# Kernel optimization log

Measured on AMD Instinct MI355X. Metric: run time of the kernel, lower is better.

Reference implementation:

```python
import jax, jax.numpy as jnp
import numpy as np
from jax import lax

EPS = 1e-3  # BatchNorm1d eps from norm_fn
SPARSE_SHAPE = (41, 200, 176)  # (z, y, x)
IN_CH = 4


def _conv3d(x, w, stride, pad):
    # x: [N,C,D,H,W], w: [O,I,kd,kh,kw]
    return lax.conv_general_dilated(x, w, window_strides=stride, padding=pad,
                                    dimension_numbers=('NCDHW', 'OIDHW', 'NCDHW'))


def _bn_relu(y, bn, mask):
    # eval-mode BatchNorm1d over active voxels == per-channel affine; inactive sites
    # must stay exactly 0 in a sparse tensor, hence the final mask multiply.
    g, b, m, v = bn[0], bn[1], bn[2], bn[3]
    scale = g * lax.rsqrt(v + EPS)
    shift = b - m * scale
    y = y * scale[None, :, None, None, None] + shift[None, :, None, None, None]
    return jax.nn.relu(y) * mask


def _subm(x, mask, w, bn):
    # SubMConv3d: conv evaluated only at existing active sites; active set unchanged.
    kd, kh, kw = w.shape[2:]
    pad = [(kd // 2, kd // 2), (kh // 2, kh // 2), (kw // 2, kw // 2)]
    return _bn_relu(_conv3d(x, w, (1, 1, 1), pad), bn, mask)


def _spconv(x, mask, w, bn, stride, pad):
    # SparseConv3d: output active set = sites with >=1 active input in receptive field.
    pads = [(p, p) for p in pad]
    y = _conv3d(x, w, stride, pads)
    k = tuple(w.shape[2:])
    new_mask = lax.reduce_window(mask, 0.0, lax.max, (1, 1) + k, (1, 1) + tuple(stride),
                                 [(0, 0), (0, 0)] + pads)
    new_mask = (new_mask > 0).astype(x.dtype)
    return _bn_relu(y, bn, new_mask), new_mask


def setup_inputs() -> dict:
    key = jax.random.key(0)
    ks = jax.random.split(key, 16)
    D, H, W = SPARSE_SHAPE
    mask = (jax.random.uniform(ks[0], (1, 1, D, H, W)) < 0.02).astype(jnp.float32)
    x = jax.random.normal(ks[1], (1, IN_CH, D, H, W), jnp.float32) * mask
    specs = [(16, IN_CH, (3, 3, 3)), (16, 16, (3, 3, 3)),
             (32, 16, (3, 3, 3)), (32, 32, (3, 3, 3)), (32, 32, (3, 3, 3)),
             (64, 32, (3, 3, 3)), (64, 64, (3, 3, 3)), (64, 64, (3, 3, 3)),
             (64, 64, (3, 3, 3)), (64, 64, (3, 3, 3)), (64, 64, (3, 3, 3)),
             (128, 64, (3, 1, 1))]
    inp = {'x': x, 'mask': mask}
    for i, (co, ci, k) in enumerate(specs):
        kk = jax.random.fold_in(ks[2], i)
        fan = ci * k[0] * k[1] * k[2]
        inp['w%d' % i] = jax.random.normal(kk, (co, ci) + k, jnp.float32) / np.sqrt(fan).astype(np.float32)
        inp['bn%d' % i] = jnp.stack([
            jax.random.uniform(jax.random.fold_in(kk, 1), (co,), minval=0.5, maxval=1.5),
            jax.random.normal(jax.random.fold_in(kk, 2), (co,)) * 0.1,
            jax.random.normal(jax.random.fold_in(kk, 3), (co,)) * 0.1,
            jax.random.uniform(jax.random.fold_in(kk, 4), (co,), minval=0.5, maxval=1.5)])
    return inp


def reference(x, mask, w0, bn0, w1, bn1, w2, bn2, w3, bn3, w4, bn4, w5, bn5,
              w6, bn6, w7, bn7, w8, bn8, w9, bn9, w10, bn10, w11, bn11):
    h = _subm(x, mask, w0, bn0)                       # conv_input (subm1)
    h = _subm(h, mask, w1, bn1)                       # conv1 -> x_conv1
    h, m2 = _spconv(h, mask, w2, bn2, (2, 2, 2), (1, 1, 1))  # conv2 down
    h = _subm(h, m2, w3, bn3)
    h = _subm(h, m2, w4, bn4)                         # x_conv2
    h, m3 = _spconv(h, m2, w5, bn5, (2, 2, 2), (1, 1, 1))    # conv3 down
    h = _subm(h, m3, w6, bn6)
    h = _subm(h, m3, w7, bn7)                         # x_conv3
    h, m4 = _spconv(h, m3, w8, bn8, (2, 2, 2), (0, 1, 1))    # conv4 down
    h = _subm(h, m4, w9, bn9)
    h = _subm(h, m4, w10, bn10)                       # x_conv4
    out, _ = _spconv(h, m4, w11, bn11, (2, 1, 1), (0, 0, 0)) # conv_out
    N, C, Dd, Hh, Ww = out.shape                      # [1,128,2,25,22]
    return out.reshape(N, C * Dd, Hh, Ww)             # spatial_features [1,256,25,22]
```

## Files before the change

kernel.cpp:

```cpp
#include <hip/hip_runtime.h>

#define BS 256

constexpr int D1=41, H1=200, W1=176; constexpr int N1v=D1*H1*W1;
constexpr int D2=21, H2=100, W2=88;  constexpr int N2v=D2*H2*W2;
constexpr int D3=11, H3=50,  W3=44;  constexpr int N3v=D3*H3*W3;
constexpr int D4=5,  H4=25,  W4=22;  constexpr int N4v=D4*H4*W4;
constexpr int DOo=2, HOo=25, WOo=22;
constexpr int ROWS1=40960;

typedef __attribute__((ext_vector_type(8))) short bf16x8;
typedef __attribute__((ext_vector_type(4))) float f32x4;

__device__ __forceinline__ float bflo(unsigned int u){ return __uint_as_float(u<<16); }
__device__ __forceinline__ float bfhi(unsigned int u){ return __uint_as_float(u & 0xffff0000u); }
__device__ __forceinline__ unsigned short f2bf(float f){
  unsigned int x = __float_as_uint(f);
  x += 0x7fffu + ((x>>16)&1u);
  return (unsigned short)(x>>16);
}
__device__ __forceinline__ void acc8(float& acc, uint4 p, const float* __restrict__ wk, int stride){
  acc = fmaf(bflo(p.x), wk[0*stride], acc);
  acc = fmaf(bfhi(p.x), wk[1*stride], acc);
  acc = fmaf(bflo(p.y), wk[2*stride], acc);
  acc = fmaf(bfhi(p.y), wk[3*stride], acc);
  acc = fmaf(bflo(p.z), wk[4*stride], acc);
  acc = fmaf(bfhi(p.z), wk[5*stride], acc);
  acc = fmaf(bflo(p.w), wk[6*stride], acc);
  acc = fmaf(bfhi(p.w), wk[7*stride], acc);
}

struct PrepArgs {
  const float* w[12]; const float* bn[12];
  void* dst[12]; float* bias[12];
  int O[12], I[12], K[12], mode[12];
  int off[13];
};

__global__ void prep_and_list_kernel(PrepArgs a, int prepB,
                                     const float* __restrict__ mask,
                                     const float* __restrict__ x,
                                     unsigned short* __restrict__ xcl,
                                     int* __restrict__ I1, int* __restrict__ list1,
                                     int* __restrict__ cnt, float* __restrict__ m2){
  if ((int)blockIdx.x < prepB){
    int t = blockIdx.x*BS + threadIdx.x;
    if (t >= a.off[12]) return;
    int li = 0;
    while (t >= a.off[li+1]) li++;
    int e = t - a.off[li];
    int O=a.O[li], I=a.I[li], K=a.K[li], mode=a.mode[li];
    const float* w = a.w[li]; const float* bn = a.bn[li];
    if (mode == 2){
      int p = e/(O*32); int rem = e - p*(O*32); int o = rem>>5; int kk = rem&31;
      int tap = 2*p + (kk>=16 ? 1 : 0); int ci = kk&15;
      float g=bn[o], b=bn[O+o], m=bn[2*O+o], v=bn[3*O+o];
      float sc = g*rsqrtf(v+1e-3f);
      float val = (tap < 27) ? w[(o*I+ci)*K + tap]*sc : 0.f;
      ((unsigned short*)a.dst[li])[e] = f2bf(val);
      if (p==0 && kk==0) a.bias[li][o] = b - m*sc;
    } else if (mode == 3){
      int ci = e % I; int tmp = e / I; int dx = tmp % 3; tmp /= 3; int o = tmp % O; int g9 = tmp / O;
      float g=bn[o], b=bn[O+o], m=bn[2*O+o], v=bn[3*O+o];
      float sc = g*rsqrtf(v+1e-3f);
      int tap = g9*3 + dx;
      ((unsigned short*)a.dst[li])[e] = f2bf(w[(o*I+ci)*27 + tap]*sc);
      if (g9==0 && dx==0 && ci==0) a.bias[li][o] = b - m*sc;
    } else {
      int k = e % K; int rest = e / K; int ci = rest % I; int o = rest / I;
      float g=bn[o], b=bn[O+o], m=bn[2*O+o], v=bn[3*O+o];
      float sc = g*rsqrtf(v+1e-3f);
      ((float*)a.dst[li])[(k*I+ci)*O + o] = w[(o*I+ci)*K + k]*sc;
      if (ci==0 && k==0) a.bias[li][o] = b - m*sc;
    }
    return;
  }
  constexpr int PER = 16;
  __shared__ int sc_[BS]; __shared__ int sbase;
  int b = blockIdx.x - prepB, t = threadIdx.x;
  int base_s = b*BS*PER;
  unsigned int bits = 0; int c = 0;
  #pragma unroll
  for (int i=0;i<PER;i++){
    int s = base_s + i*BS + t;
    bool act = false;
    if (s < N1v){
      act = mask[s] > 0.f;
      unsigned short h0 = f2bf(x[s]),       h1 = f2bf(x[N1v+s]);
      unsigned short h2 = f2bf(x[2*N1v+s]), h3 = f2bf(x[3*N1v+s]);
      uint2 pk; pk.x = ((unsigned)h1<<16)|h0; pk.y = ((unsigned)h3<<16)|h2;
      *(uint2*)(xcl + (size_t)s*4) = pk;
    }
    bits |= (act?1u:0u) << i; c += act;
  }
  sc_[t] = c;
  __syncthreads();
  for (int ofs=1; ofs<BS; ofs<<=1){
    int v = (t>=ofs) ? sc_[t-ofs] : 0;
    __syncthreads();
    sc_[t] += v;
    __syncthreads();
  }
  if (t == BS-1) sbase = atomicAdd(cnt, sc_[t]);
  __syncthreads();
  int pos = sbase + sc_[t] - c;
  #pragma unroll
  for (int i=0;i<PER;i++){
    if (bits & (1u<<i)){
      int s = base_s + i*BS + t;
      list1[pos] = s; I1[s] = pos+1; pos++;
      int zz = s/(H1*W1); int rem = s - zz*(H1*W1); int yy = rem/W1; int xx = rem - yy*W1;
      int az = zz+1, ay = yy+1, ax = xx+1;
      int zlo = (az-2) <= 0 ? 0 : (az-1)/2;  int zhi = min(D2-1, az/2);
      int ylo = (ay-2) <= 0 ? 0 : (ay-1)/2;  int yhi = min(H2-1, ay/2);
      int xlo = (ax-2) <= 0 ? 0 : (ax-1)/2;  int xhi = min(W2-1, ax/2);
      for (int zo=zlo; zo<=zhi; zo++)
        for (int yo=ylo; yo<=yhi; yo++)
          for (int xo=xlo; xo<=xhi; xo++)
            m2[(zo*H2+yo)*W2+xo] = 1.f;
    }
  }
}

template<int N,int HI,int WI,int DON,int HON,int WON,int PZ,int PY,int PX,bool SCAT>
__global__ void compact_mask_kernel(const float* __restrict__ mout,
                                    int* __restrict__ list, int* __restrict__ cnt1,
                                    float* __restrict__ mnext){
  __shared__ int sc[BS]; __shared__ int sbase;
  int b = blockIdx.x, t = threadIdx.x;
  int s = b*BS + t;
  bool act = (s < N) && (mout[s] > 0.f);
  int c = act ? 1 : 0;
  sc[t] = c;
  __syncthreads();
  for (int ofs=1; ofs<BS; ofs<<=1){
    int v = (t>=ofs) ? sc[t-ofs] : 0;
    __syncthreads();
    sc[t] += v;
    __syncthreads();
  }
  if (t == BS-1) sbase = atomicAdd(cnt1, sc[t]);
  __syncthreads();
  if (act){
    list[sbase + sc[t] - 1] = s;
    if (SCAT){
      int zz = s/(HI*WI); int rem = s - zz*(HI*WI); int yy = rem/WI; int xx = rem - yy*WI;
      int az = zz+PZ, ay = yy+PY, ax = xx+PX;
      int zlo = (az-2) <= 0 ? 0 : (az-1)/2;  int zhi = min(DON-1, az/2);
      int ylo = (ay-2) <= 0 ? 0 : (ay-1)/2;  int yhi = min(HON-1, ay/2);
      int xlo = (ax-2) <= 0 ? 0 : (ax-1)/2;  int xhi = min(WON-1, ax/2);
      for (int zo=zlo; zo<=zhi; zo++)
        for (int yo=ylo; yo<=yhi; yo++)
          for (int xo=xlo; xo<=xhi; xo++)
            mnext[(zo*HON+yo)*WON+xo] = 1.f;
    }
  }
}

__global__ void subm_l0_kernel(const unsigned short* __restrict__ xcl,
                               const int* __restrict__ list1, const int* __restrict__ cnt,
                               const float* __restrict__ wt, const float* __restrict__ bias,
                               unsigned short* __restrict__ fout){
  __shared__ float Wl[27*4*16];
  __shared__ float Bl[16];
  int t = threadIdx.x;
  for (int e=t; e<27*4*16; e+=BS) Wl[e] = wt[e];
  if (t < 16) Bl[t] = bias[t];
  __syncthreads();
  int row = blockIdx.x*BS + t;
  if (row >= cnt[0]) return;
  int s = list1[row];
  int z = s/(H1*W1); int r = s - z*(H1*W1); int y = r/W1; int xx = r - y*W1;
  float acc[16];
  #pragma unroll
  for (int o=0;o<16;o++) acc[o] = Bl[o];
  #pragma unroll
  for (int dz=-1; dz<=1; dz++){ int zz=z+dz; if ((unsigned)zz >= (unsigned)D1) continue;
    #pragma unroll
    for (int dy=-1; dy<=1; dy++){ int yy=y+dy; if ((unsigned)yy >= (unsigned)H1) continue;
      #pragma unroll
      for (int dx=-1; dx<=1; dx++){ int xc=xx+dx; if ((unsigned)xc >= (unsigned)W1) continue;
        int ns = (zz*H1+yy)*W1+xc;
        int k = ((dz+1)*3+(dy+1))*3+(dx+1);
        uint2 pk = *(const uint2*)(xcl + (size_t)ns*4);
        float x0 = bflo(pk.x), x1 = bfhi(pk.x), x2 = bflo(pk.y), x3 = bfhi(pk.y);
        const float* wk = Wl + k*64;
        #pragma unroll
        for (int o=0;o<16;o++)
          acc[o] = fmaf(x0, wk[o], fmaf(x1, wk[16+o], fmaf(x2, wk[32+o], fmaf(x3, wk[48+o], acc[o]))));
      }}}
  #pragma unroll
  for (int o=0;o<16;o++) fout[row*16+o] = f2bf(fmaxf(acc[o], 0.f));
}

template<int COUT,int HO,int WO,int PZ,int PY,int PX,int STR,bool DENSE_OUT>
__global__ __launch_bounds__(256)
void conv_mfma_l1_kernel(const unsigned short* __restrict__ fin,
                         const int* __restrict__ I1,
                         const int* __restrict__ list, const int* __restrict__ cnt, int cidx,
                         const unsigned short* __restrict__ wbt,
                         const float* __restrict__ bias,
                         unsigned short* __restrict__ outp){
  constexpr int BP = 40;
  constexpr int NT = COUT/16;
  __shared__ __align__(16) unsigned short B[14*COUT*BP];

  int nrows = cnt[cidx];
  int row0 = blockIdx.x*64;
  if (row0 >= nrows) return;

  int t = threadIdx.x;
  int lane = t & 63, wave = t >> 6;
  int m = lane & 15, quad = lane >> 4;

  constexpr int TOT = 14*COUT*32;
  for (int e = t*8; e < TOT; e += BS*8){
    int n = e >> 5, c = e & 31;
    *(uint4*)(&B[n*BP + c]) = *(const uint4*)(wbt + e);
  }

  int row = row0 + wave*16 + m;
  bool rv = row < nrows;
  int z=0, y=0, x=0;
  {
    int s = list[rv ? row : row0];
    z = s/(HO*WO); int rem = s - z*(HO*WO); y = rem/WO; x = rem - y*WO;
  }

  int rr[14];
  #pragma unroll
  for (int p=0;p<14;p++){
    int tap = 2*p + (quad>>1);
    rr[p] = 0;
    if (rv && tap < 27){
      int dz = tap/9, rem = tap - dz*9, dy = rem/3, dx = rem - dy*3;
      int zz = STR*z - PZ + dz, yy = STR*y - PY + dy, xx = STR*x - PX + dx;
      if ((unsigned)zz < (unsigned)D1 && (unsigned)yy < (unsigned)H1 && (unsigned)xx < (unsigned)W1)
        rr[p] = I1[(zz*H1+yy)*W1+xx];
    }
  }
  __syncthreads();

  f32x4 acc[NT];
  #pragma unroll
  for (int i=0;i<NT;i++) acc[i] = (f32x4){0.f,0.f,0.f,0.f};

  bf16x8 acur = (bf16x8){0,0,0,0,0,0,0,0};
  if (rr[0] > 0) acur = *(const bf16x8*)(fin + (size_t)(rr[0]-1)*16 + (quad&1)*8);
  #pragma unroll
  for (int p=0;p<14;p++){
    bf16x8 anext = (bf16x8){0,0,0,0,0,0,0,0};
    if (p < 13 && rr[p+1] > 0)
      anext = *(const bf16x8*)(fin + (size_t)(rr[p+1]-1)*16 + (quad&1)*8);
    #pragma unroll
    for (int nt=0; nt<NT; nt++){
      bf16x8 b = *(const bf16x8*)(&B[(p*COUT + nt*16 + m)*BP + quad*8]);
      acc[nt] = __builtin_amdgcn_mfma_f32_16x16x32_bf16(acur, b, acc[nt], 0, 0, 0);
    }
    acur = anext;
  }

  #pragma unroll
  for (int nt=0; nt<NT; nt++){
    int cout = nt*16 + m;
    float bv = bias[cout];
    #pragma unroll
    for (int rg=0; rg<4; rg++){
      int rw = row0 + wave*16 + quad*4 + rg;
      if (rw < nrows){
        float v = fmaxf(acc[nt][rg] + bv, 0.f);
        if (DENSE_OUT){
          int s = list[rw];
          outp[(size_t)s*COUT + cout] = f2bf(v);
        } else {
          outp[(size_t)rw*COUT + cout] = f2bf(v);
        }
      }
    }
  }
}

template<int CIN,int COUT,int DI,int HI,int WI,int HO,int WO,int PZ,int PY,int PX,int STR>
__global__ __launch_bounds__(256)
void conv_mfma2_kernel(const unsigned short* __restrict__ gin,
                       const int* __restrict__ list, const int* __restrict__ cnt, int cidx,
                       const unsigned short* __restrict__ wg,
                       const float* __restrict__ bias,
                       unsigned short* __restrict__ gout){
  constexpr int KW = 3*CIN;
  constexpr int BP = KW + 8;
  constexpr int NT = COUT/16;
  constexpr int KT = KW/32;
  constexpr int PREN = (COUT*KW + BS*8 - 1)/(BS*8);
  __shared__ __align__(16) unsigned short B[2][COUT*BP];

  int nrows = cnt[cidx];
  int row0 = blockIdx.x*64;
  if (row0 >= nrows) return;

  int t = threadIdx.x;
  int lane = t & 63, wave = t >> 6;
  int m = lane & 15, quad = lane >> 4;

  #pragma unroll
  for (int i=0;i<PREN;i++){
    int e = t*8 + i*BS*8;
    if (e < COUT*KW){
      int n = e / KW, c = e - n*KW;
      *(uint4*)(&B[0][n*BP + c]) = *(const uint4*)(wg + e);
    }
  }

  int row = row0 + wave*16 + m;
  bool rv = row < nrows;
  int z=0, y=0, x=0;
  {
    int s = list[rv ? row : row0];
    z = s/(HO*WO); int rem = s - z*(HO*WO); y = rem/WO; x = rem - y*WO;
  }

  auto loadA = [&](int g, bf16x8* av){
    int dz = g/3, dy = g - dz*3;
    int zz = STR*z - PZ + dz, yy = STR*y - PY + dy, xx0 = STR*x - PX;
    bool zyok = rv && (unsigned)zz < (unsigned)DI && (unsigned)yy < (unsigned)HI;
    int base = ((zz*HI + yy)*WI + xx0)*CIN;
    #pragma unroll
    for (int kt=0; kt<KT; kt++){
      int tapx = (kt*32)/CIN;
      av[kt] = (bf16x8){0,0,0,0,0,0,0,0};
      if (zyok && (unsigned)(xx0 + tapx) < (unsigned)WI)
        av[kt] = *(const bf16x8*)(gin + (size_t)(base + kt*32 + quad*8));
    }
  };

  f32x4 acc[NT];
  #pragma unroll
  for (int i=0;i<NT;i++) acc[i] = (f32x4){0.f,0.f,0.f,0.f};

  bf16x8 acur[KT], anext[KT];
  loadA(0, acur);
  __syncthreads();

  #pragma unroll
  for (int g=0; g<9; g++){
    uint4 pre[PREN];
    if (g < 8){
      const unsigned short* src = wg + (size_t)(g+1)*COUT*KW;
      #pragma unroll
      for (int i=0;i<PREN;i++){
        int e = t*8 + i*BS*8;
        pre[i] = (e < COUT*KW) ? *(const uint4*)(src + e) : (uint4){0,0,0,0};
      }
      loadA(g+1, anext);
    }
    #pragma unroll
    for (int kt=0; kt<KT; kt++){
      #pragma unroll
      for (int nt=0; nt<NT; nt++){
        bf16x8 b = *(const bf16x8*)(&B[g&1][(nt*16 + m)*BP + kt*32 + quad*8]);
        acc[nt] = __builtin_amdgcn_mfma_f32_16x16x32_bf16(acur[kt], b, acc[nt], 0, 0, 0);
      }
    }
    if (g < 8){
      #pragma unroll
      for (int i=0;i<PREN;i++){
        int e = t*8 + i*BS*8;
        if (e < COUT*KW){
          int n = e / KW, c = e - n*KW;
          *(uint4*)(&B[(g+1)&1][n*BP + c]) = pre[i];
        }
      }
      #pragma unroll
      for (int kt=0; kt<KT; kt++) acur[kt] = anext[kt];
    }
    __syncthreads();
  }

  #pragma unroll
  for (int nt=0; nt<NT; nt++){
    int cout = nt*16 + m;
    float bv = bias[cout];
    #pragma unroll
    for (int rg=0; rg<4; rg++){
      int rw = row0 + wave*16 + quad*4 + rg;
      if (rw < nrows){
        int s = list[rw];
        gout[(size_t)s*COUT + cout] = f2bf(fmaxf(acc[nt][rg] + bv, 0.f));
      }
    }
  }
}

template<int CIN,int COUT,int DI,int HI,int WI,int HO,int WO,int PZ,int PY,int PX,int STR>
__global__ __launch_bounds__(256)
void conv_tp_kernel(const unsigned short* __restrict__ gin,
                    const int* __restrict__ list, const int* __restrict__ cnt, int cidx,
                    const unsigned short* __restrict__ wg,
                    const float* __restrict__ bias,
                    unsigned short* __restrict__ gout){
  constexpr int KW = 3*CIN;
  constexpr int NT = COUT/16;
  constexpr int KT = KW/32;
  __shared__ float R[4][NT*256];

  int nrows = cnt[cidx];
  int row0 = blockIdx.x*16;
  if (row0 >= nrows) return;

  int t = threadIdx.x;
  int lane = t & 63, wave = t >> 6;
  int m = lane & 15, quad = lane >> 4;

  int row = row0 + m;
  bool rv = row < nrows;
  int z=0, y=0, x=0;
  {
    int s = list[rv ? row : row0];
    z = s/(HO*WO); int rem = s - z*(HO*WO); y = rem/WO; x = rem - y*WO;
  }

  bf16x8 av[3][KT];
  #pragma unroll
  for (int i=0;i<3;i++){
    int g = wave + i*4;
    #pragma unroll
    for (int kt=0; kt<KT; kt++) av[i][kt] = (bf16x8){0,0,0,0,0,0,0,0};
    if (g < 9){
      int dz = g/3, dy = g - dz*3;
      int zz = STR*z - PZ + dz, yy = STR*y - PY + dy, xx0 = STR*x - PX;
      bool zyok = rv && (unsigned)zz < (unsigned)DI && (unsigned)yy < (unsigned)HI;
      int base = ((zz*HI + yy)*WI + xx0)*CIN;
      #pragma unroll
      for (int kt=0; kt<KT; kt++){
        int tapx = (kt*32)/CIN;
        if (zyok && (unsigned)(xx0 + tapx) < (unsigned)WI)
          av[i][kt] = *(const bf16x8*)(gin + (size_t)(base + kt*32 + quad*8));
      }
    }
  }

  f32x4 acc[NT];
  #pragma unroll
  for (int i=0;i<NT;i++) acc[i] = (f32x4){0.f,0.f,0.f,0.f};

  #pragma unroll
  for (int i=0;i<3;i++){
    int g = wave + i*4;
    if (g < 9){
      const unsigned short* wsrc = wg + (size_t)g*COUT*KW;
      #pragma unroll
      for (int kt=0; kt<KT; kt++){
        #pragma unroll
        for (int nt=0; nt<NT; nt++){
          bf16x8 b = *(const bf16x8*)(wsrc + (size_t)(nt*16 + m)*KW + kt*32 + quad*8);
          acc[nt] = __builtin_amdgcn_mfma_f32_16x16x32_bf16(av[i][kt], b, acc[nt], 0, 0, 0);
        }
      }
    }
  }

  #pragma unroll
  for (int nt=0; nt<NT; nt++)
    #pragma unroll
    for (int rg=0; rg<4; rg++)
      R[wave][nt*256 + (quad*4+rg)*16 + m] = acc[nt][rg];
  __syncthreads();

  for (int e = t; e < 16*COUT; e += BS){
    int r = e / COUT, cout = e % COUT;
    int nt = cout >> 4, mm = cout & 15;
    int idx = nt*256 + r*16 + mm;
    float sum = R[0][idx] + R[1][idx] + R[2][idx] + R[3][idx];
    int rw = row0 + r;
    if (rw < nrows){
      int s = list[rw];
      gout[(size_t)s*COUT + cout] = f2bf(fmaxf(sum + bias[cout], 0.f));
    }
  }
}

__global__ void conv_out_kernel(const unsigned short* __restrict__ g4,
                                const float* __restrict__ m4,
                                const float* __restrict__ wt, const float* __restrict__ bias,
                                float* __restrict__ out){
  int t = blockIdx.x*BS + threadIdx.x;
  if (t >= 128*DOo*HOo*WOo) return;
  int cout = t & 127; int s = t >> 7;
  int d = s/(HOo*WOo); int r = s - d*(HOo*WOo); int h = r/WOo; int w = r - h*WOo;
  float res = 0.f;
  bool act = false;
  float acc = bias[cout];
  for (int dz=0; dz<3; dz++){
    int z4 = 2*d + dz;
    int site = (z4*H4 + h)*W4 + w;
    if (m4[site] == 0.f) continue;
    act = true;
    const uint4* fr = (const uint4*)(g4 + (size_t)site*64);
    const float* wk = wt + dz*64*128 + cout;
    #pragma unroll
    for (int q=0; q<8; q++) acc8(acc, fr[q], wk + q*8*128, 128);
  }
  if (act) res = fmaxf(acc, 0.f);
  out[((cout*DOo + d)*HOo + h)*WOo + w] = res;
}

extern "C" void kernel_launch(void* const* d_in, const int* in_sizes, int n_in,
                              void* d_out, int out_size, void* d_ws, size_t ws_size,
                              hipStream_t stream){
  const float* x    = (const float*)d_in[0];
  const float* mask = (const float*)d_in[1];
  const float* w[12]; const float* bnp[12];
  for (int i=0;i<12;i++){ w[i]=(const float*)d_in[2+2*i]; bnp[i]=(const float*)d_in[3+2*i]; }

  char* base = (char*)d_ws; size_t off = 0;
  auto alloc = [&](size_t b)->void*{ void* p = base + off; off = (off + b + 255) & ~(size_t)255; return p; };

  int* cnt   = (int*)alloc(16);
  int* I1    = (int*)alloc((size_t)N1v*4);
  unsigned short* g2a = (unsigned short*)alloc((size_t)N2v*32*2);
  unsigned short* g2b = (unsigned short*)alloc((size_t)N2v*32*2);
  unsigned short* g3a = (unsigned short*)alloc((size_t)N3v*64*2);
  unsigned short* g3b = (unsigned short*)alloc((size_t)N3v*64*2);
  unsigned short* g4a = (unsigned short*)alloc((size_t)N4v*64*2);
  unsigned short* g4b = (unsigned short*)alloc((size_t)N4v*64*2);
  float* m2 = (float*)alloc((size_t)N2v*4);
  float* m3 = (float*)alloc((size_t)N3v*4);
  float* m4 = (float*)alloc((size_t)N4v*4);
  size_t zero_bytes = off;
  unsigned short* xcl = (unsigned short*)alloc((size_t)N1v*4*2);
  int* list1 = (int*)alloc((size_t)ROWS1*4);
  unsigned short* f1a = (unsigned short*)alloc((size_t)ROWS1*16*2);
  unsigned short* f1b = (unsigned short*)alloc((size_t)ROWS1*16*2);
  int* list2 = (int*)alloc((size_t)N2v*4);
  int* list3 = (int*)alloc((size_t)N3v*4);
  int* list4 = (int*)alloc((size_t)N4v*4);

  static const int Oa[12]={16,16,32,32,32,64,64,64,64,64,64,128};
  static const int Ia[12]={ 4,16,16,32,32,32,64,64,64,64,64, 64};
  static const int Ka[12]={27,27,27,27,27,27,27,27,27,27,27,  3};
  static const int Ma[12]={ 0, 2, 2, 3, 3, 3, 3, 3, 3, 3, 3,  0};
  float* wt[12]; float* bs[12]; unsigned short* wbt[12];
  for (int i=0;i<12;i++){
    bs[i] = (float*)alloc((size_t)Oa[i]*4);
    wt[i]=nullptr; wbt[i]=nullptr;
    if (Ma[i]==0)      wt[i]  = (float*)alloc((size_t)Oa[i]*Ia[i]*Ka[i]*4);
    else if (Ma[i]==3) wbt[i] = (unsigned short*)alloc((size_t)Oa[i]*Ia[i]*27*2);
    else               wbt[i] = (unsigned short*)alloc((size_t)14*Oa[i]*32*2);
  }

  hipMemsetAsync(base, 0, zero_bytes, stream);

  PrepArgs pa;
  pa.off[0] = 0;
  for (int i=0;i<12;i++){
    pa.w[i]=w[i]; pa.bn[i]=bnp[i]; pa.bias[i]=bs[i];
    pa.O[i]=Oa[i]; pa.I[i]=Ia[i]; pa.K[i]=Ka[i]; pa.mode[i]=Ma[i];
    pa.dst[i] = (Ma[i]==0) ? (void*)wt[i] : (void*)wbt[i];
    int tot = (Ma[i]==2) ? 14*Oa[i]*32 : Oa[i]*Ia[i]*Ka[i];
    pa.off[i+1] = pa.off[i] + tot;
  }
  int prepB = (pa.off[12]+BS-1)/BS;
  int listB = (N1v + BS*16 - 1)/(BS*16);
  prep_and_list_kernel<<<prepB + listB, BS, 0, stream>>>(pa, prepB, mask, x, xcl, I1, list1, cnt, m2);

  subm_l0_kernel<<<(ROWS1+BS-1)/BS, BS, 0, stream>>>(xcl, list1, cnt, wt[0], bs[0], f1a);
  conv_mfma_l1_kernel<16,H1,W1,1,1,1,1,false><<<ROWS1/64, 256, 0, stream>>>
      (f1a, I1, list1, cnt, 0, wbt[1], bs[1], f1b);

  compact_mask_kernel<N2v,H2,W2,D3,H3,W3,1,1,1,true><<<(N2v+BS-1)/BS, BS, 0, stream>>>(m2, list2, cnt+1, m3);
  conv_mfma_l1_kernel<32,H2,W2,1,1,1,2,true><<<(N2v+63)/64, 256, 0, stream>>>
      (f1b, I1, list2, cnt, 1, wbt[2], bs[2], g2a);

  {
    int nb = (N2v + 63)/64;
    conv_mfma2_kernel<32,32,D2,H2,W2,H2,W2,1,1,1,1><<<nb, 256, 0, stream>>>(g2a, list2, cnt, 1, wbt[3], bs[3], g2b);
    conv_mfma2_kernel<32,32,D2,H2,W2,H2,W2,1,1,1,1><<<nb, 256, 0, stream>>>(g2b, list2, cnt, 1, wbt[4], bs[4], g2a);
  }

  compact_mask_kernel<N3v,H3,W3,D4,H4,W4,0,1,1,true><<<(N3v+BS-1)/BS, BS, 0, stream>>>(m3, list3, cnt+2, m4);
  {
    conv_tp_kernel<32,64,D2,H2,W2,H3,W3,1,1,1,2><<<(N3v+15)/16, 256, 0, stream>>>(g2a, list3, cnt, 2, wbt[5], bs[5], g3a);
    int nb = (N3v + 63)/64;
    conv_mfma2_kernel<64,64,D3,H3,W3,H3,W3,1,1,1,1><<<nb, 256, 0, stream>>>(g3a, list3, cnt, 2, wbt[6], bs[6], g3b);
    conv_mfma2_kernel<64,64,D3,H3,W3,H3,W3,1,1,1,1><<<nb, 256, 0, stream>>>(g3b, list3, cnt, 2, wbt[7], bs[7], g3a);
  }

  compact_mask_kernel<N4v,H4,W4,1,1,1,0,0,0,false><<<(N4v+BS-1)/BS, BS, 0, stream>>>(m4, list4, cnt+3, nullptr);
  {
    int nb = (N4v + 15)/16;
    conv_tp_kernel<64,64,D3,H3,W3,H4,W4,0,1,1,2><<<nb, 256, 0, stream>>>(g3a, list4, cnt, 3, wbt[8], bs[8], g4a);
    conv_tp_kernel<64,64,D4,H4,W4,H4,W4,1,1,1,1><<<nb, 256, 0, stream>>>(g4a, list4, cnt, 3, wbt[9], bs[9], g4b);
    conv_tp_kernel<64,64,D4,H4,W4,H4,W4,1,1,1,1><<<nb, 256, 0, stream>>>(g4b, list4, cnt, 3, wbt[10], bs[10], g4a);
  }

  conv_out_kernel<<<(128*DOo*HOo*WOo)/BS, BS, 0, stream>>>(g4a, m4, wt[11], bs[11], (float*)d_out);
}
```

Before: 360.5 us.

## Use single-wave blocks with register-streamed weights for early sparse convs

Replaces the 256-thread MFMA conv kernels for layers 1-4 with 64-thread single-wave kernels that each process 16 rows. Weight fragments come straight from global memory (through cache) into registers and are double-buffered, so the shared-memory weight staging and the __syncthreads are gone. The aim is to drop the per-block LDS fill cost and give finer-grained blocks for sparse, variable row counts. In exchange, every wave reloads the full weights from cache, many more blocks are launched, and register pressure rises from the double buffers.

```diff
diff --git a/kernel.cpp b/kernel.cpp
--- a/kernel.cpp
+++ b/kernel.cpp
@@ -194,32 +194,22 @@
 }
 
 template<int COUT,int HO,int WO,int PZ,int PY,int PX,int STR,bool DENSE_OUT>
-__global__ __launch_bounds__(256)
-void conv_mfma_l1_kernel(const unsigned short* __restrict__ fin,
-                         const int* __restrict__ I1,
-                         const int* __restrict__ list, const int* __restrict__ cnt, int cidx,
-                         const unsigned short* __restrict__ wbt,
-                         const float* __restrict__ bias,
-                         unsigned short* __restrict__ outp){
-  constexpr int BP = 40;
+__global__ __launch_bounds__(64)
+void conv_w1_kernel(const unsigned short* __restrict__ fin,
+                    const int* __restrict__ I1,
+                    const int* __restrict__ list, const int* __restrict__ cnt, int cidx,
+                    const unsigned short* __restrict__ wbt,
+                    const float* __restrict__ bias,
+                    unsigned short* __restrict__ outp){
   constexpr int NT = COUT/16;
-  __shared__ __align__(16) unsigned short B[14*COUT*BP];
-
   int nrows = cnt[cidx];
-  int row0 = blockIdx.x*64;
+  int row0 = blockIdx.x*16;
   if (row0 >= nrows) return;
 
-  int t = threadIdx.x;
-  int lane = t & 63, wave = t >> 6;
+  int lane = threadIdx.x;
   int m = lane & 15, quad = lane >> 4;
 
-  constexpr int TOT = 14*COUT*32;
-  for (int e = t*8; e < TOT; e += BS*8){
-    int n = e >> 5, c = e & 31;
-    *(uint4*)(&B[n*BP + c]) = *(const uint4*)(wbt + e);
-  }
-
-  int row = row0 + wave*16 + m;
+  int row = row0 + m;
   bool rv = row < nrows;
   int z=0, y=0, x=0;
   {
@@ -239,7 +229,6 @@
         rr[p] = I1[(zz*H1+yy)*W1+xx];
     }
   }
-  __syncthreads();
 
   f32x4 acc[NT];
   #pragma unroll
@@ -247,17 +236,30 @@
 
   bf16x8 acur = (bf16x8){0,0,0,0,0,0,0,0};
   if (rr[0] > 0) acur = *(const bf16x8*)(fin + (size_t)(rr[0]-1)*16 + (quad&1)*8);
+  bf16x8 bcur[NT];
+  #pragma unroll
+  for (int nt=0; nt<NT; nt++)
+    bcur[nt] = *(const bf16x8*)(wbt + (size_t)(nt*16 + m)*32 + quad*8);
+
   #pragma unroll
   for (int p=0;p<14;p++){
     bf16x8 anext = (bf16x8){0,0,0,0,0,0,0,0};
-    if (p < 13 && rr[p+1] > 0)
-      anext = *(const bf16x8*)(fin + (size_t)(rr[p+1]-1)*16 + (quad&1)*8);
-    #pragma unroll
-    for (int nt=0; nt<NT; nt++){
-      bf16x8 b = *(const bf16x8*)(&B[(p*COUT + nt*16 + m)*BP + quad*8]);
-      acc[nt] = __builtin_amdgcn_mfma_f32_16x16x32_bf16(acur, b, acc[nt], 0, 0, 0);
-    }
-    acur = anext;
+    bf16x8 bnext[NT];
+    if (p < 13){
+      if (rr[p+1] > 0)
+        anext = *(const bf16x8*)(fin + (size_t)(rr[p+1]-1)*16 + (quad&1)*8);
+      #pragma unroll
+      for (int nt=0; nt<NT; nt++)
+        bnext[nt] = *(const bf16x8*)(wbt + (size_t)((p+1)*COUT + nt*16 + m)*32 + quad*8);
+    }
+    #pragma unroll
+    for (int nt=0; nt<NT; nt++)
+      acc[nt] = __builtin_amdgcn_mfma_f32_16x16x32_bf16(acur, bcur[nt], acc[nt], 0, 0, 0);
+    if (p < 13){
+      acur = anext;
+      #pragma unroll
+      for (int nt=0; nt<NT; nt++) bcur[nt] = bnext[nt];
+    }
   }
 
   #pragma unroll
@@ -266,7 +268,7 @@
     float bv = bias[cout];
     #pragma unroll
     for (int rg=0; rg<4; rg++){
-      int rw = row0 + wave*16 + quad*4 + rg;
+      int rw = row0 + quad*4 + rg;
       if (rw < nrows){
         float v = fmaxf(acc[nt][rg] + bv, 0.f);
         if (DENSE_OUT){
@@ -275,6 +277,93 @@
         } else {
           outp[(size_t)rw*COUT + cout] = f2bf(v);
         }
+      }
+    }
+  }
+}
+
+template<int CIN,int COUT,int DI,int HI,int WI,int PZ,int PY,int PX>
+__global__ __launch_bounds__(64)
+void conv_w2_kernel(const unsigned short* __restrict__ gin,
+                    const int* __restrict__ list, const int* __restrict__ cnt, int cidx,
+                    const unsigned short* __restrict__ wg,
+                    const float* __restrict__ bias,
+                    unsigned short* __restrict__ gout){
+  constexpr int KW = 3*CIN;
+  constexpr int NT = COUT/16;
+  constexpr int KT = KW/32;
+  int nrows = cnt[cidx];
+  int row0 = blockIdx.x*16;
+  if (row0 >= nrows) return;
+
+  int lane = threadIdx.x;
+  int m = lane & 15, quad = lane >> 4;
+
+  int row = row0 + m;
+  bool rv = row < nrows;
+  int z=0, y=0, x=0;
+  {
+    int s = list[rv ? row : row0];
+    z = s/(HI*WI); int rem = s - z*(HI*WI); y = rem/WI; x = rem - y*WI;
+  }
+
+  auto loadA = [&](int g, bf16x8* av){
+    int dz = g/3, dy = g - dz*3;
+    int zz = z - PZ + dz, yy = y - PY + dy, xx0 = x - PX;
+    bool zyok = rv && (unsigned)zz < (unsigned)DI && (unsigned)yy < (unsigned)HI;
+    int base = ((zz*HI + yy)*WI + xx0)*CIN;
+    #pragma unroll
+    for (int kt=0; kt<KT; kt++){
+      int tapx = (kt*32)/CIN;
+      av[kt] = (bf16x8){0,0,0,0,0,0,0,0};
+      if (zyok && (unsigned)(xx0 + tapx) < (unsigned)WI)
+        av[kt] = *(const bf16x8*)(gin + (size_t)(base + kt*32 + quad*8));
+    }
+  };
+  auto loadB = [&](int g, bf16x8 bv[KT][NT]){
+    const unsigned short* src = wg + (size_t)g*COUT*KW;
+    #pragma unroll
+    for (int kt=0; kt<KT; kt++)
+      #pragma unroll
+      for (int nt=0; nt<NT; nt++)
+        bv[kt][nt] = *(const bf16x8*)(src + (size_t)(nt*16 + m)*KW + kt*32 + quad*8);
+  };
+
+  f32x4 acc[NT];
+  #pragma unroll
+  for (int i=0;i<NT;i++) acc[i] = (f32x4){0.f,0.f,0.f,0.f};
+
+  bf16x8 a0[KT], a1[KT], b0[KT][NT], b1[KT][NT];
+  loadA(0, a0); loadB(0, b0);
+
+  #pragma unroll
+  for (int g=0; g<9; g++){
+    if (g < 8){ loadA(g+1, a1); loadB(g+1, b1); }
+    #pragma unroll
+    for (int kt=0; kt<KT; kt++)
+      #pragma unroll
+      for (int nt=0; nt<NT; nt++)
+        acc[nt] = __builtin_amdgcn_mfma_f32_16x16x32_bf16(a0[kt], b0[kt][nt], acc[nt], 0, 0, 0);
+    if (g < 8){
+      #pragma unroll
+      for (int kt=0; kt<KT; kt++){
+        a0[kt] = a1[kt];
+        #pragma unroll
+        for (int nt=0; nt<NT; nt++) b0[kt][nt] = b1[kt][nt];
+      }
+    }
+  }
+
+  #pragma unroll
+  for (int nt=0; nt<NT; nt++){
+    int cout = nt*16 + m;
+    float bv = bias[cout];
+    #pragma unroll
+    for (int rg=0; rg<4; rg++){
+      int rw = row0 + quad*4 + rg;
+      if (rw < nrows){
+        int s = list[rw];
+        gout[(size_t)s*COUT + cout] = f2bf(fmaxf(acc[nt][rg] + bv, 0.f));
       }
     }
   }
@@ -564,17 +653,17 @@
   prep_and_list_kernel<<<prepB + listB, BS, 0, stream>>>(pa, prepB, mask, x, xcl, I1, list1, cnt, m2);
 
   subm_l0_kernel<<<(ROWS1+BS-1)/BS, BS, 0, stream>>>(xcl, list1, cnt, wt[0], bs[0], f1a);
-  conv_mfma_l1_kernel<16,H1,W1,1,1,1,1,false><<<ROWS1/64, 256, 0, stream>>>
+  conv_w1_kernel<16,H1,W1,1,1,1,1,false><<<ROWS1/16, 64, 0, stream>>>
       (f1a, I1, list1, cnt, 0, wbt[1], bs[1], f1b);
 
   compact_mask_kernel<N2v,H2,W2,D3,H3,W3,1,1,1,true><<<(N2v+BS-1)/BS, BS, 0, stream>>>(m2, list2, cnt+1, m3);
-  conv_mfma_l1_kernel<32,H2,W2,1,1,1,2,true><<<(N2v+63)/64, 256, 0, stream>>>
+  conv_w1_kernel<32,H2,W2,1,1,1,2,true><<<(N2v+15)/16, 64, 0, stream>>>
       (f1b, I1, list2, cnt, 1, wbt[2], bs[2], g2a);
 
   {
-    int nb = (N2v + 63)/64;
-    conv_mfma2_kernel<32,32,D2,H2,W2,H2,W2,1,1,1,1><<<nb, 256, 0, stream>>>(g2a, list2, cnt, 1, wbt[3], bs[3], g2b);
-    conv_mfma2_kernel<32,32,D2,H2,W2,H2,W2,1,1,1,1><<<nb, 256, 0, stream>>>(g2b, list2, cnt, 1, wbt[4], bs[4], g2a);
+    int nb = (N2v + 15)/16;
+    conv_w2_kernel<32,32,D2,H2,W2,1,1,1><<<nb, 64, 0, stream>>>(g2a, list2, cnt, 1, wbt[3], bs[3], g2b);
+    conv_w2_kernel<32,32,D2,H2,W2,1,1,1><<<nb, 64, 0, stream>>>(g2b, list2, cnt, 1, wbt[4], bs[4], g2a);
   }
 
   compact_mask_kernel<N3v,H3,W3,D4,H4,W4,0,1,1,true><<<(N3v+BS-1)/BS, BS, 0, stream>>>(m3, list3, cnt+2, m4);
```

Measured after the change: 384.7 us. +6.7%, slower.

## Split conv taps across waves with LDS reduction for level-1/2 convs

Applied to the files above, without the earlier changes.

Replaces the level-1 MFMA conv, which staged weights in LDS and computed 64 rows per block, with a tap-parallel variant. Each of the 4 waves handles a quarter of the kernel taps for 16 rows, loading weights straight from global memory. Partial sums are then reduced through shared memory before bias, ReLU and store. The level-2 submanifold convs also switch from conv_mfma2_kernel to the existing conv_tp_kernel with 16-row blocks. This trades weight-staging cost and serial tap latency for more blocks, an extra LDS reduction, and repeated global weight loads.

```diff
diff --git a/kernel.cpp b/kernel.cpp
--- a/kernel.cpp
+++ b/kernel.cpp
@@ -195,31 +195,23 @@
 
 template<int COUT,int HO,int WO,int PZ,int PY,int PX,int STR,bool DENSE_OUT>
 __global__ __launch_bounds__(256)
-void conv_mfma_l1_kernel(const unsigned short* __restrict__ fin,
-                         const int* __restrict__ I1,
-                         const int* __restrict__ list, const int* __restrict__ cnt, int cidx,
-                         const unsigned short* __restrict__ wbt,
-                         const float* __restrict__ bias,
-                         unsigned short* __restrict__ outp){
-  constexpr int BP = 40;
+void conv_tp_l1_kernel(const unsigned short* __restrict__ fin,
+                       const int* __restrict__ I1,
+                       const int* __restrict__ list, const int* __restrict__ cnt, int cidx,
+                       const unsigned short* __restrict__ wbt,
+                       const float* __restrict__ bias,
+                       unsigned short* __restrict__ outp){
   constexpr int NT = COUT/16;
-  __shared__ __align__(16) unsigned short B[14*COUT*BP];
-
+  __shared__ float R[4][NT*256];
   int nrows = cnt[cidx];
-  int row0 = blockIdx.x*64;
+  int row0 = blockIdx.x*16;
   if (row0 >= nrows) return;
 
   int t = threadIdx.x;
   int lane = t & 63, wave = t >> 6;
   int m = lane & 15, quad = lane >> 4;
 
-  constexpr int TOT = 14*COUT*32;
-  for (int e = t*8; e < TOT; e += BS*8){
-    int n = e >> 5, c = e & 31;
-    *(uint4*)(&B[n*BP + c]) = *(const uint4*)(wbt + e);
-  }
-
-  int row = row0 + wave*16 + m;
+  int row = row0 + m;
   bool rv = row < nrows;
   int z=0, y=0, x=0;
   {
@@ -227,54 +219,69 @@
     z = s/(HO*WO); int rem = s - z*(HO*WO); y = rem/WO; x = rem - y*WO;
   }
 
-  int rr[14];
-  #pragma unroll
-  for (int p=0;p<14;p++){
-    int tap = 2*p + (quad>>1);
-    rr[p] = 0;
-    if (rv && tap < 27){
-      int dz = tap/9, rem = tap - dz*9, dy = rem/3, dx = rem - dy*3;
-      int zz = STR*z - PZ + dz, yy = STR*y - PY + dy, xx = STR*x - PX + dx;
-      if ((unsigned)zz < (unsigned)D1 && (unsigned)yy < (unsigned)H1 && (unsigned)xx < (unsigned)W1)
-        rr[p] = I1[(zz*H1+yy)*W1+xx];
-    }
-  }
-  __syncthreads();
+  int rr[4];
+  #pragma unroll
+  for (int i=0;i<4;i++){
+    int p = wave + i*4;
+    rr[i] = 0;
+    if (p < 14){
+      int tap = 2*p + (quad>>1);
+      if (rv && tap < 27){
+        int dz = tap/9, rem = tap - dz*9, dy = rem/3, dx = rem - dy*3;
+        int zz = STR*z - PZ + dz, yy = STR*y - PY + dy, xx = STR*x - PX + dx;
+        if ((unsigned)zz < (unsigned)D1 && (unsigned)yy < (unsigned)H1 && (unsigned)xx < (unsigned)W1)
+          rr[i] = I1[(zz*H1+yy)*W1+xx];
+      }
+    }
+  }
+  bf16x8 av[4]; bf16x8 bv[4][NT];
+  #pragma unroll
+  for (int i=0;i<4;i++){
+    int p = wave + i*4;
+    av[i] = (bf16x8){0,0,0,0,0,0,0,0};
+    if (rr[i] > 0) av[i] = *(const bf16x8*)(fin + (size_t)(rr[i]-1)*16 + (quad&1)*8);
+    #pragma unroll
+    for (int nt=0; nt<NT; nt++){
+      bv[i][nt] = (bf16x8){0,0,0,0,0,0,0,0};
+      if (p < 14)
+        bv[i][nt] = *(const bf16x8*)(wbt + (size_t)(p*COUT + nt*16 + m)*32 + quad*8);
+    }
+  }
 
   f32x4 acc[NT];
   #pragma unroll
   for (int i=0;i<NT;i++) acc[i] = (f32x4){0.f,0.f,0.f,0.f};
 
-  bf16x8 acur = (bf16x8){0,0,0,0,0,0,0,0};
-  if (rr[0] > 0) acur = *(const bf16x8*)(fin + (size_t)(rr[0]-1)*16 + (quad&1)*8);
-  #pragma unroll
-  for (int p=0;p<14;p++){
-    bf16x8 anext = (bf16x8){0,0,0,0,0,0,0,0};
-    if (p < 13 && rr[p+1] > 0)
-      anext = *(const bf16x8*)(fin + (size_t)(rr[p+1]-1)*16 + (quad&1)*8);
-    #pragma unroll
-    for (int nt=0; nt<NT; nt++){
-      bf16x8 b = *(const bf16x8*)(&B[(p*COUT + nt*16 + m)*BP + quad*8]);
-      acc[nt] = __builtin_amdgcn_mfma_f32_16x16x32_bf16(acur, b, acc[nt], 0, 0, 0);
-    }
-    acur = anext;
-  }
-
-  #pragma unroll
-  for (int nt=0; nt<NT; nt++){
-    int cout = nt*16 + m;
-    float bv = bias[cout];
-    #pragma unroll
-    for (int rg=0; rg<4; rg++){
-      int rw = row0 + wave*16 + quad*4 + rg;
-      if (rw < nrows){
-        float v = fmaxf(acc[nt][rg] + bv, 0.f);
-        if (DENSE_OUT){
-          int s = list[rw];
-          outp[(size_t)s*COUT + cout] = f2bf(v);
-        } else {
-          outp[(size_t)rw*COUT + cout] = f2bf(v);
-        }
+  #pragma unroll
+  for (int i=0;i<4;i++){
+    int p = wave + i*4;
+    if (p < 14){
+      #pragma unroll
+      for (int nt=0; nt<NT; nt++)
+        acc[nt] = __builtin_amdgcn_mfma_f32_16x16x32_bf16(av[i], bv[i][nt], acc[nt], 0, 0, 0);
+    }
+  }
+
+  #pragma unroll
+  for (int nt=0; nt<NT; nt++)
+    #pragma unroll
+    for (int rg=0; rg<4; rg++)
+      R[wave][nt*256 + (quad*4+rg)*16 + m] = acc[nt][rg];
+  __syncthreads();
+
+  for (int e = t; e < 16*COUT; e += BS){
+    int r = e / COUT, cout = e % COUT;
+    int nt = cout >> 4, mm = cout & 15;
+    int idx = nt*256 + r*16 + mm;
+    float sum = R[0][idx] + R[1][idx] + R[2][idx] + R[3][idx];
+    int rw = row0 + r;
+    if (rw < nrows){
+      float v = fmaxf(sum + bias[cout], 0.f);
+      if (DENSE_OUT){
+        int s = list[rw];
+        outp[(size_t)s*COUT + cout] = f2bf(v);
+      } else {
+        outp[(size_t)rw*COUT + cout] = f2bf(v);
       }
     }
   }
@@ -564,17 +571,17 @@
   prep_and_list_kernel<<<prepB + listB, BS, 0, stream>>>(pa, prepB, mask, x, xcl, I1, list1, cnt, m2);
 
   subm_l0_kernel<<<(ROWS1+BS-1)/BS, BS, 0, stream>>>(xcl, list1, cnt, wt[0], bs[0], f1a);
-  conv_mfma_l1_kernel<16,H1,W1,1,1,1,1,false><<<ROWS1/64, 256, 0, stream>>>
+  conv_tp_l1_kernel<16,H1,W1,1,1,1,1,false><<<(ROWS1+15)/16, 256, 0, stream>>>
       (f1a, I1, list1, cnt, 0, wbt[1], bs[1], f1b);
 
   compact_mask_kernel<N2v,H2,W2,D3,H3,W3,1,1,1,true><<<(N2v+BS-1)/BS, BS, 0, stream>>>(m2, list2, cnt+1, m3);
-  conv_mfma_l1_kernel<32,H2,W2,1,1,1,2,true><<<(N2v+63)/64, 256, 0, stream>>>
+  conv_tp_l1_kernel<32,H2,W2,1,1,1,2,true><<<(N2v+15)/16, 256, 0, stream>>>
       (f1b, I1, list2, cnt, 1, wbt[2], bs[2], g2a);
 
   {
-    int nb = (N2v + 63)/64;
-    conv_mfma2_kernel<32,32,D2,H2,W2,H2,W2,1,1,1,1><<<nb, 256, 0, stream>>>(g2a, list2, cnt, 1, wbt[3], bs[3], g2b);
-    conv_mfma2_kernel<32,32,D2,H2,W2,H2,W2,1,1,1,1><<<nb, 256, 0, stream>>>(g2b, list2, cnt, 1, wbt[4], bs[4], g2a);
+    int nb = (N2v + 15)/16;
+    conv_tp_kernel<32,32,D2,H2,W2,H2,W2,1,1,1,1><<<nb, 256, 0, stream>>>(g2a, list2, cnt, 1, wbt[3], bs[3], g2b);
+    conv_tp_kernel<32,32,D2,H2,W2,H2,W2,1,1,1,1><<<nb, 256, 0, stream>>>(g2b, list2, cnt, 1, wbt[4], bs[4], g2a);
   }
 
   compact_mask_kernel<N3v,H3,W3,D4,H4,W4,0,1,1,true><<<(N3v+BS-1)/BS, BS, 0, stream>>>(m3, list3, cnt+2, m4);
```

Measured after the change: 384.6 us. 6.7% more time.

## Fuse tail stages into one persistent kernel with grid barriers

Applied to the files above, without the earlier changes.

Replaces the last five launches (mask compaction, three layer-4 convolutions and conv_out) with a single persistent kernel of 256 blocks. The stages are separated by atomic-counter grid barriers, and each conv phase loops over its tiles in grid-stride fashion. The aim is to remove launch overhead and inter-kernel gaps on the small tail layers. In exchange it adds spin-wait barrier cost, and it depends on all 256 blocks being co-resident; otherwise the grid deadlocks.

```diff
diff --git a/kernel.cpp b/kernel.cpp
--- a/kernel.cpp
+++ b/kernel.cpp
@@ -479,29 +479,167 @@
   }
 }
 
-__global__ void conv_out_kernel(const unsigned short* __restrict__ g4,
-                                const float* __restrict__ m4,
-                                const float* __restrict__ wt, const float* __restrict__ bias,
-                                float* __restrict__ out){
-  int t = blockIdx.x*BS + threadIdx.x;
-  if (t >= 128*DOo*HOo*WOo) return;
-  int cout = t & 127; int s = t >> 7;
-  int d = s/(HOo*WOo); int r = s - d*(HOo*WOo); int h = r/WOo; int w = r - h*WOo;
-  float res = 0.f;
-  bool act = false;
-  float acc = bias[cout];
-  for (int dz=0; dz<3; dz++){
-    int z4 = 2*d + dz;
-    int site = (z4*H4 + h)*W4 + w;
-    if (m4[site] == 0.f) continue;
-    act = true;
-    const uint4* fr = (const uint4*)(g4 + (size_t)site*64);
-    const float* wk = wt + dz*64*128 + cout;
-    #pragma unroll
-    for (int q=0; q<8; q++) acc8(acc, fr[q], wk + q*8*128, 128);
-  }
-  if (act) res = fmaxf(acc, 0.f);
-  out[((cout*DOo + d)*HOo + h)*WOo + w] = res;
+__device__ __forceinline__ void gbar(int* bar, int target){
+  __threadfence();
+  __syncthreads();
+  if (threadIdx.x == 0){
+    __hip_atomic_fetch_add(bar, 1, __ATOMIC_ACQ_REL, __HIP_MEMORY_SCOPE_AGENT);
+    while (__hip_atomic_load(bar, __ATOMIC_ACQUIRE, __HIP_MEMORY_SCOPE_AGENT) < target)
+      __builtin_amdgcn_s_sleep(10);
+  }
+  __syncthreads();
+  __threadfence();
+}
+
+template<int CIN,int COUT,int DI,int HI,int WI,int HO,int WO,int PZ,int PY,int PX,int STR>
+__device__ __forceinline__
+void tp_phase(const unsigned short* __restrict__ gin,
+              const int* __restrict__ list, int nrows,
+              const unsigned short* __restrict__ wg,
+              const float* __restrict__ bias,
+              unsigned short* __restrict__ gout,
+              float* __restrict__ Rl){
+  constexpr int KW = 3*CIN;
+  constexpr int NT = COUT/16;
+  constexpr int KT = KW/32;
+  int t = threadIdx.x;
+  int lane = t & 63, wave = t >> 6;
+  int m = lane & 15, quad = lane >> 4;
+  int ntiles = (nrows + 15)/16;
+  for (int tile = blockIdx.x; tile < ntiles; tile += gridDim.x){
+    int row0 = tile*16;
+    int row = row0 + m;
+    bool rv = row < nrows;
+    int z=0, y=0, x=0;
+    {
+      int s = list[rv ? row : row0];
+      z = s/(HO*WO); int rem = s - z*(HO*WO); y = rem/WO; x = rem - y*WO;
+    }
+    bf16x8 av[3][KT];
+    #pragma unroll
+    for (int i=0;i<3;i++){
+      int g = wave + i*4;
+      #pragma unroll
+      for (int kt=0; kt<KT; kt++) av[i][kt] = (bf16x8){0,0,0,0,0,0,0,0};
+      if (g < 9){
+        int dz = g/3, dy = g - dz*3;
+        int zz = STR*z - PZ + dz, yy = STR*y - PY + dy, xx0 = STR*x - PX;
+        bool zyok = rv && (unsigned)zz < (unsigned)DI && (unsigned)yy < (unsigned)HI;
+        int base = ((zz*HI + yy)*WI + xx0)*CIN;
+        #pragma unroll
+        for (int kt=0; kt<KT; kt++){
+          int tapx = (kt*32)/CIN;
+          if (zyok && (unsigned)(xx0 + tapx) < (unsigned)WI)
+            av[i][kt] = *(const bf16x8*)(gin + (size_t)(base + kt*32 + quad*8));
+        }
+      }
+    }
+    f32x4 acc[NT];
+    #pragma unroll
+    for (int i=0;i<NT;i++) acc[i] = (f32x4){0.f,0.f,0.f,0.f};
+    #pragma unroll
+    for (int i=0;i<3;i++){
+      int g = wave + i*4;
+      if (g < 9){
+        const unsigned short* wsrc = wg + (size_t)g*COUT*KW;
+        #pragma unroll
+        for (int kt=0; kt<KT; kt++){
+          #pragma unroll
+          for (int nt=0; nt<NT; nt++){
+            bf16x8 b = *(const bf16x8*)(wsrc + (size_t)(nt*16 + m)*KW + kt*32 + quad*8);
+            acc[nt] = __builtin_amdgcn_mfma_f32_16x16x32_bf16(av[i][kt], b, acc[nt], 0, 0, 0);
+          }
+        }
+      }
+    }
+    #pragma unroll
+    for (int nt=0; nt<NT; nt++)
+      #pragma unroll
+      for (int rg=0; rg<4; rg++)
+        Rl[wave*(NT*256) + nt*256 + (quad*4+rg)*16 + m] = acc[nt][rg];
+    __syncthreads();
+    for (int e = t; e < 16*COUT; e += BS){
+      int r = e / COUT, cout = e % COUT;
+      int nt = cout >> 4, mm = cout & 15;
+      int idx = nt*256 + r*16 + mm;
+      float sum = Rl[0*(NT*256)+idx] + Rl[1*(NT*256)+idx] + Rl[2*(NT*256)+idx] + Rl[3*(NT*256)+idx];
+      int rw = row0 + r;
+      if (rw < nrows){
+        int s = list[rw];
+        gout[(size_t)s*COUT + cout] = f2bf(fmaxf(sum + bias[cout], 0.f));
+      }
+    }
+    __syncthreads();
+  }
+}
+
+__global__ __launch_bounds__(256)
+void tail_kernel(const float* __restrict__ m4,
+                 int* __restrict__ list4, int* __restrict__ cnt,
+                 const unsigned short* __restrict__ g3a,
+                 unsigned short* __restrict__ g4a, unsigned short* __restrict__ g4b,
+                 const unsigned short* __restrict__ w8, const float* __restrict__ b8,
+                 const unsigned short* __restrict__ w9, const float* __restrict__ b9,
+                 const unsigned short* __restrict__ w10, const float* __restrict__ b10,
+                 const float* __restrict__ wt11, const float* __restrict__ bs11,
+                 float* __restrict__ out){
+  __shared__ float Rl[4*4*256];
+  __shared__ int sc[BS]; __shared__ int sbase;
+  int t = threadIdx.x;
+  int nb = gridDim.x;
+
+  {
+    int nch = (N4v + BS - 1)/BS;
+    for (int ch = blockIdx.x; ch < nch; ch += nb){
+      int s = ch*BS + t;
+      bool act = (s < N4v) && (m4[s] > 0.f);
+      int c = act ? 1 : 0;
+      sc[t] = c;
+      __syncthreads();
+      for (int ofs=1; ofs<BS; ofs<<=1){
+        int v = (t>=ofs) ? sc[t-ofs] : 0;
+        __syncthreads();
+        sc[t] += v;
+        __syncthreads();
+      }
+      if (t == BS-1) sbase = atomicAdd(cnt+3, sc[t]);
+      __syncthreads();
+      if (act) list4[sbase + sc[t] - 1] = s;
+      __syncthreads();
+    }
+  }
+  gbar(cnt+4, 1*nb);
+  int nrows = cnt[3];
+
+  tp_phase<64,64,D3,H3,W3,H4,W4,0,1,1,2>(g3a, list4, nrows, w8, b8, g4a, Rl);
+  gbar(cnt+4, 2*nb);
+  tp_phase<64,64,D4,H4,W4,H4,W4,1,1,1,1>(g4a, list4, nrows, w9, b9, g4b, Rl);
+  gbar(cnt+4, 3*nb);
+  tp_phase<64,64,D4,H4,W4,H4,W4,1,1,1,1>(g4b, list4, nrows, w10, b10, g4a, Rl);
+  gbar(cnt+4, 4*nb);
+
+  {
+    int total = 128*DOo*HOo*WOo;
+    for (int e = blockIdx.x*BS + t; e < total; e += nb*BS){
+      int cout = e & 127; int s = e >> 7;
+      int d = s/(HOo*WOo); int r = s - d*(HOo*WOo); int h = r/WOo; int w = r - h*WOo;
+      float res = 0.f;
+      bool act = false;
+      float acc = bs11[cout];
+      for (int dz=0; dz<3; dz++){
+        int z4 = 2*d + dz;
+        int site = (z4*H4 + h)*W4 + w;
+        if (m4[site] == 0.f) continue;
+        act = true;
+        const uint4* fr = (const uint4*)(g4a + (size_t)site*64);
+        const float* wk = wt11 + dz*64*128 + cout;
+        #pragma unroll
+        for (int q=0; q<8; q++) acc8(acc, fr[q], wk + q*8*128, 128);
+      }
+      if (act) res = fmaxf(acc, 0.f);
+      out[((cout*DOo + d)*HOo + h)*WOo + w] = res;
+    }
+  }
 }
 
 extern "C" void kernel_launch(void* const* d_in, const int* in_sizes, int n_in,
@@ -515,7 +653,7 @@
   char* base = (char*)d_ws; size_t off = 0;
   auto alloc = [&](size_t b)->void*{ void* p = base + off; off = (off + b + 255) & ~(size_t)255; return p; };
 
-  int* cnt   = (int*)alloc(16);
+  int* cnt   = (int*)alloc(32);
   int* I1    = (int*)alloc((size_t)N1v*4);
   unsigned short* g2a = (unsigned short*)alloc((size_t)N2v*32*2);
   unsigned short* g2b = (unsigned short*)alloc((size_t)N2v*32*2);
@@ -585,13 +723,7 @@
     conv_mfma2_kernel<64,64,D3,H3,W3,H3,W3,1,1,1,1><<<nb, 256, 0, stream>>>(g3b, list3, cnt, 2, wbt[7], bs[7], g3a);
   }
 
-  compact_mask_kernel<N4v,H4,W4,1,1,1,0,0,0,false><<<(N4v+BS-1)/BS, BS, 0, stream>>>(m4, list4, cnt+3, nullptr);
-  {
-    int nb = (N4v + 15)/16;
-    conv_tp_kernel<64,64,D3,H3,W3,H4,W4,0,1,1,2><<<nb, 256, 0, stream>>>(g3a, list4, cnt, 3, wbt[8], bs[8], g4a);
-    conv_tp_kernel<64,64,D4,H4,W4,H4,W4,1,1,1,1><<<nb, 256, 0, stream>>>(g4a, list4, cnt, 3, wbt[9], bs[9], g4b);
-    conv_tp_kernel<64,64,D4,H4,W4,H4,W4,1,1,1,1><<<nb, 256, 0, stream>>>(g4b, list4, cnt, 3, wbt[10], bs[10], g4a);
-  }
-
-  conv_out_kernel<<<(128*DOo*HOo*WOo)/BS, BS, 0, stream>>>(g4a, m4, wt[11], bs[11], (float*)d_out);
-}
+  tail_kernel<<<256, 256, 0, stream>>>(m4, list4, cnt, g3a, g4a, g4b,
+                                       wbt[8], bs[8], wbt[9], bs[9], wbt[10], bs[10],
+                                       wt[11], bs[11], (float*)d_out);
+}
```

Measured after the change: 625.2 us. 73.4% more time.
